# Optimization experiments

Hardware: AMD Instinct MI355X
Metric: run time of the kernel (lower is better)

## Reference

```python
import jax, jax.numpy as jnp
import numpy as np

B, T, C = 4, 2048, 1024  # n_embd == input_size == 1024
H, D = 16, 64            # num_heads, head_size


def setup_inputs() -> dict:
    key = jax.random.key(0)
    ks = jax.random.split(key, 5)
    s_in = (1.0 / C) ** 0.5   # ~Linear default init scale
    s_pr = (1.0 / (H * D)) ** 0.5
    return {
        "x": jax.random.normal(ks[0], (B, T, C), dtype=jnp.float32),
        "wq": jax.random.normal(ks[1], (H, C, D), dtype=jnp.float32) * s_in,
        "wk": jax.random.normal(ks[2], (H, C, D), dtype=jnp.float32) * s_in,
        "wv": jax.random.normal(ks[3], (H, C, D), dtype=jnp.float32) * s_in,
        "w_proj": jax.random.normal(ks[4], (H * D, C), dtype=jnp.float32) * s_pr,
        "b_proj": jnp.zeros((C,), dtype=jnp.float32),
    }


def reference(x, wq, wk, wv, w_proj, b_proj):
    Bb, Tt, Cc = x.shape
    # Batched per-head projections: [B,T,C] x [H,C,D] -> [B,H,T,D]
    q = jnp.einsum("btc,hcd->bhtd", x, wq)
    k = jnp.einsum("btc,hcd->bhtd", x, wk)
    v = jnp.einsum("btc,hcd->bhtd", x, wv)
    # NOTE: original scales by C**-0.5 with C = full embedding dim (quirk preserved)
    scale = Cc ** (-0.5)
    scores = jnp.einsum("bhtd,bhsd->bhts", q, k) * scale  # [B,H,T,T]
    causal = jnp.tril(jnp.ones((Tt, Tt), dtype=bool))
    scores = jnp.where(causal, scores, -jnp.inf)
    wei = jax.nn.softmax(scores, axis=-1)
    out = jnp.einsum("bhts,bhsd->bhtd", wei, v)           # [B,H,T,D]
    out = out.transpose(0, 2, 1, 3).reshape(Bb, Tt, -1)    # concat heads [B,T,H*D]
    return out @ w_proj + b_proj                           # [B,T,C]
```

## Files before the change

### kernel.cpp

```cpp
#include <hip/hip_runtime.h>
#include <stdint.h>


typedef uint32_t u32;
typedef __bf16 bf16x8 __attribute__((ext_vector_type(8)));
typedef __bf16 bf16x4 __attribute__((ext_vector_type(4)));
typedef unsigned short us8 __attribute__((ext_vector_type(8)));
typedef float f32x4 __attribute__((ext_vector_type(4)));

#define EXP2F(x) __builtin_amdgcn_exp2f(x)

static __device__ __forceinline__ unsigned short f2bf(float f) {
  union { float f; u32 i; } cv; cv.f = f;
  u32 x = cv.i;
  u32 r = (x + 0x7fffu + ((x >> 16) & 1u)) >> 16;
  return (unsigned short)r;
}

static __device__ __forceinline__ void gload_lds16(const unsigned short* g, unsigned short* l) {
  __builtin_amdgcn_global_load_lds(
      (__attribute__((address_space(1))) u32*)g,
      (__attribute__((address_space(3))) u32*)l, 16, 0, 0);
}

#define G8_LGKM do { asm volatile("s_waitcnt lgkmcnt(0)" ::: "memory"); \
                     __builtin_amdgcn_sched_barrier(0); } while (0)

__global__ __launch_bounds__(256) void cvt_f32_bf16(
    const float* __restrict__ src, unsigned short* __restrict__ dst) {
  size_t i = (size_t)(blockIdx.x * 256 + threadIdx.x) * 8u;
  float4 a = *(const float4*)(src + i);
  float4 b = *(const float4*)(src + i + 4);
  us8 v;
  v[0] = f2bf(a.x); v[1] = f2bf(a.y); v[2] = f2bf(a.z); v[3] = f2bf(a.w);
  v[4] = f2bf(b.x); v[5] = f2bf(b.y); v[6] = f2bf(b.z); v[7] = f2bf(b.w);
  *(us8*)(dst + i) = v;
}

__global__ __launch_bounds__(256) void transpose_qkv(
    const float* __restrict__ wq, const float* __restrict__ wk,
    const float* __restrict__ wv, unsigned short* __restrict__ dst) {
  __shared__ unsigned short lds[64][66];
  const float* src = (blockIdx.z == 0) ? wq : (blockIdx.z == 1) ? wk : wv;
  unsigned short* d = dst + ((size_t)blockIdx.z << 20);
  const int tid = threadIdx.x;
  const int h = blockIdx.y, c0 = blockIdx.x * 64;
  const float* s = src + (size_t)h * 65536u + (size_t)c0 * 64u;
#pragma unroll
  for (int it = 0; it < 16; ++it) {
    int idx = it * 256 + tid;
    int r = idx >> 6, dd = idx & 63;
    lds[dd][r] = f2bf(s[r * 64 + dd]);
  }
  __syncthreads();
#pragma unroll
  for (int it = 0; it < 16; ++it) {
    int idx = it * 256 + tid;
    int dd = idx >> 6, r = idx & 63;
    d[(size_t)(h * 64 + dd) * 1024u + c0 + r] = lds[dd][r];
  }
}

__global__ __launch_bounds__(256) void transpose_proj(
    const float* __restrict__ wp, unsigned short* __restrict__ dst) {
  __shared__ unsigned short lds[64][66];
  const int tid = threadIdx.x;
  const int c0 = blockIdx.x * 64, r0 = blockIdx.y * 64;
#pragma unroll
  for (int it = 0; it < 16; ++it) {
    int idx = it * 256 + tid;
    int r = idx >> 6, cc = idx & 63;
    lds[cc][r] = f2bf(wp[(size_t)(r0 + r) * 1024u + c0 + cc]);
  }
  __syncthreads();
#pragma unroll
  for (int it = 0; it < 16; ++it) {
    int idx = it * 256 + tid;
    int cc = idx >> 6, r = idx & 63;
    dst[(size_t)(c0 + cc) * 1024u + r0 + r] = lds[cc][r];
  }
}

__global__ __launch_bounds__(256) void transpose_v(
    const unsigned short* __restrict__ v, unsigned short* __restrict__ vt) {
  __shared__ unsigned short lds[64][66];
  const int tid = threadIdx.x;
  const int bh = blockIdx.y, t0 = blockIdx.x * 64;
  const unsigned short* src = v + ((size_t)(bh >> 4) * 2048 + t0) * 1024u + (bh & 15) * 64;
  unsigned short* dst = vt + (size_t)bh * 131072u + t0;
#pragma unroll
  for (int it = 0; it < 16; ++it) {
    int idx = it * 256 + tid;
    int r = idx >> 6, dd = idx & 63;
    lds[dd][r] = src[(size_t)r * 1024u + dd];
  }
  __syncthreads();
#pragma unroll
  for (int it = 0; it < 16; ++it) {
    int idx = it * 256 + tid;
    int dd = idx >> 6, r = idx & 63;
    dst[(size_t)dd * 2048u + r] = lds[dd][r];
  }
}

static __device__ __forceinline__ void gn_stage(const unsigned short* g,
                                                unsigned short* d, int tid) {
#pragma unroll
  for (int l = 0; l < 2; ++l) {
    int cid = l * 512 + tid;
    int r = cid >> 3, c = cid & 7;
    gload_lds16(g + (size_t)r * 1024 + ((c ^ (r & 7)) << 3), d + cid * 8);
  }
}
static __device__ __forceinline__ void gn_ldA(bf16x8 af[4][2], const unsigned short* As,
                                              int wr, int l15, int lhi) {
#pragma unroll
  for (int mi = 0; mi < 4; ++mi)
#pragma unroll
    for (int ks = 0; ks < 2; ++ks) {
      int row = wr * 64 + mi * 16 + l15;
      af[mi][ks] = *(const bf16x8*)(As + row * 64 + ((((ks << 2) | lhi) ^ (row & 7)) << 3));
    }
}
static __device__ __forceinline__ void gn_ldB(bf16x8 bf[2][2], const unsigned short* Bs,
                                              int wc, int np, int l15, int lhi) {
#pragma unroll
  for (int ni = 0; ni < 2; ++ni)
#pragma unroll
    for (int ks = 0; ks < 2; ++ks) {
      int row = wc * 64 + np * 32 + ni * 16 + l15;
      bf[ni][ks] = *(const bf16x8*)(Bs + row * 64 + ((((ks << 2) | lhi) ^ (row & 7)) << 3));
    }
}
static __device__ __forceinline__ void gn_quad(f32x4 acc[4][4], bf16x8 af[4][2],
                                               bf16x8 bf[2][2], int np) {
#pragma unroll
  for (int ks = 0; ks < 2; ++ks)
#pragma unroll
    for (int mi = 0; mi < 4; ++mi)
#pragma unroll
      for (int ni = 0; ni < 2; ++ni)
        acc[mi][np * 2 + ni] = __builtin_amdgcn_mfma_f32_16x16x32_bf16(
            af[mi][ks], bf[ni][ks], acc[mi][np * 2 + ni], 0, 0, 0);
}

template <int F32OUT>
__global__ __launch_bounds__(512, 2) void gemmN(
    const unsigned short* __restrict__ A, const unsigned short* __restrict__ Bt,
    const float* __restrict__ bias, void* __restrict__ Cv) {
  extern __shared__ __align__(16) unsigned short ldsm[];
  unsigned short* Ab = ldsm;
  unsigned short* Bb = ldsm + 16384;
  const int tid = threadIdx.x, wid = tid >> 6, lane = tid & 63;
  const int l15 = lane & 15, lhi = lane >> 4;
  const int wr = wid >> 2, wc = wid & 3;
  const int bid = blockIdx.x;
  const int mt = ((bid & 7) << 3) | ((bid >> 3) & 7);
  const int nt = bid >> 6;
  const int m0 = mt * 128, n0 = nt * 256;
  const unsigned short* Ag = A + (size_t)m0 * 1024;
  const unsigned short* Bg = Bt + (size_t)n0 * 1024;

  f32x4 acc[4][4] = {};
  bf16x8 af[4][2], b0[2][2], b1[2][2];

  gn_stage(Bg, Bb, tid);
  gn_stage(Bg + 128 * 1024, Bb + 8192, tid);
  gn_stage(Ag, Ab, tid);
  gn_stage(Ag + 64, Ab + 8192, tid);
  asm volatile("s_waitcnt vmcnt(2)" ::: "memory");
  __builtin_amdgcn_s_barrier();

  for (int j = 0; j < 8; ++j) {
    const bool last = (j == 7);
    const int kc = j * 128;
    gn_ldA(af, Ab, wr, l15, lhi);
    gn_ldB(b0, Bb, wc, 0, l15, lhi);
    gn_stage(Bg + (kc + 64), Bb + 16384, tid);
    gn_stage(Bg + 128 * 1024 + (kc + 64), Bb + 24576, tid);
    __builtin_amdgcn_s_barrier(); G8_LGKM;
    __builtin_amdgcn_s_setprio(1); gn_quad(acc, af, b0, 0); __builtin_amdgcn_s_setprio(0);
    __builtin_amdgcn_s_barrier();
    gn_ldB(b1, Bb, wc, 1, l15, lhi);
    if (!last) gn_stage(Ag + (kc + 128), Ab, tid);
    __builtin_amdgcn_s_barrier(); G8_LGKM;
    __builtin_amdgcn_s_setprio(1); gn_quad(acc, af, b1, 1); __builtin_amdgcn_s_setprio(0);
    if (last) { asm volatile("s_waitcnt vmcnt(0)" ::: "memory"); }
    else      { asm volatile("s_waitcnt vmcnt(2)" ::: "memory"); }
    __builtin_amdgcn_s_barrier();
    gn_ldA(af, Ab + 8192, wr, l15, lhi);
    gn_ldB(b0, Bb + 16384, wc, 0, l15, lhi);
    if (!last) {
      gn_stage(Bg + (kc + 128), Bb, tid);
      gn_stage(Bg + 128 * 1024 + (kc + 128), Bb + 8192, tid);
    }
    __builtin_amdgcn_s_barrier(); G8_LGKM;
    __builtin_amdgcn_s_setprio(1); gn_quad(acc, af, b0, 0); __builtin_amdgcn_s_setprio(0);
    __builtin_amdgcn_s_barrier();
    gn_ldB(b1, Bb + 16384, wc, 1, l15, lhi);
    if (!last) gn_stage(Ag + (kc + 192), Ab + 8192, tid);
    __builtin_amdgcn_s_barrier(); G8_LGKM;
    __builtin_amdgcn_s_setprio(1); gn_quad(acc, af, b1, 1); __builtin_amdgcn_s_setprio(0);
    if (!last) asm volatile("s_waitcnt vmcnt(2)" ::: "memory");
    __builtin_amdgcn_s_barrier();
  }

#pragma unroll
  for (int mi = 0; mi < 4; ++mi) {
#pragma unroll
    for (int ni = 0; ni < 4; ++ni) {
      const int n = n0 + wc * 64 + ni * 16 + l15;
      const int mr = m0 + wr * 64 + mi * 16 + lhi * 4;
      if constexpr (F32OUT) {
        float* O = (float*)Cv;
        const float b = bias[n];
#pragma unroll
        for (int r = 0; r < 4; ++r)
          O[(size_t)(mr + r) * 1024 + n] = acc[mi][ni][r] + b;
      } else {
        unsigned short* O = (unsigned short*)Cv + ((size_t)(n >> 10) << 23);
        const int nc = n & 1023;
#pragma unroll
        for (int r = 0; r < 4; ++r)
          O[(size_t)(mr + r) * 1024 + nc] = f2bf(acc[mi][ni][r]);
      }
    }
  }
}

#define QT 128
#define KVT 64
#define PSTR 72
#define SCLOG2E 0.04508422f
#define DTHR 128.0f

__global__ __launch_bounds__(512, 4) void attn_fwd(
    const unsigned short* __restrict__ Qg, const unsigned short* __restrict__ Kg,
    const unsigned short* __restrict__ Vtg, unsigned short* __restrict__ Og) {
  __shared__ __align__(16) unsigned short Kl[2][64 * 64];
  __shared__ __align__(16) unsigned short Vl[2][64 * 64];
  __shared__ __align__(16) unsigned short Pl[8][16 * PSTR];
  const int tid = threadIdx.x, wid = tid >> 6, lane = tid & 63;
  const int l15 = lane & 15, lhi = lane >> 4, x7 = lane & 7;
  const int bid = blockIdx.x;
  const int sub = bid & 63, pair = bid >> 6;
  const int bh = ((sub & 7) << 3) | (sub >> 3);
  const int qtA = pair, qtB = 15 - pair;
  const int n0 = 2 * (qtA + 1), n1 = 2 * (qtB + 1);
  const int ntot = n0 + n1;
  const size_t base = (size_t)(bh >> 4) * (2048u * 1024u) + (size_t)(bh & 15) * 64u;
  const size_t vtbase = (size_t)bh * 131072u;

  auto s0_of = [&](int g) { return ((g < n0) ? g : g - n0) * KVT; };

  auto stage = [&](int bufi, int s0) {
    int q = tid;
    int r = q >> 3;
    int c = (q & 7) ^ (r & 7);
    gload_lds16(Kg + base + (size_t)(s0 + r) * 1024u + c * 8, &Kl[bufi][q * 8]);
    gload_lds16(Vtg + vtbase + (size_t)r * 2048u + s0 + c * 8, &Vl[bufi][q * 8]);
  };

  stage(0, 0);
  __syncthreads();

  int g = 0;
  for (int pass = 0; pass < 2; ++pass) {
    const int qt = pass ? qtB : qtA;
    const int nt = pass ? n1 : n0;
    const int qrow0 = qt * QT + wid * 16;

    bf16x8 qf[2];
#pragma unroll
    for (int kj = 0; kj < 2; ++kj)
      qf[kj] = *(const bf16x8*)(Qg + base +
          (size_t)(qrow0 + l15) * 1024u + kj * 32 + lhi * 8);

    float mrun = -1e30f, lrun = 0.0f;
    f32x4 oacc[4] = {};

    for (int kt = 0; kt < nt; ++kt, ++g) {
      const int cur = g & 1;
      const int s0 = kt * KVT;
      if (g + 1 < ntot) stage(cur ^ 1, s0_of(g + 1));
      if (s0 <= qrow0 + 15) {
        const bool notfull = (s0 + KVT - 1 > qrow0);
        const unsigned short* Kb = Kl[cur];
        const unsigned short* Vb = Vl[cur];

        f32x4 sacc[4] = {};
#pragma unroll
        for (int kj = 0; kj < 2; ++kj) {
          bf16x8 kf[4];
#pragma unroll
          for (int sj = 0; sj < 4; ++sj) {
            int r = sj * 16 + l15;
            kf[sj] = *(const bf16x8*)(&Kb[r * 64 + (((kj * 4 + lhi) ^ x7) * 8)]);
          }
#pragma unroll
          for (int sj = 0; sj < 4; ++sj)
            sacc[sj] = __builtin_amdgcn_mfma_f32_16x16x32_bf16(
                kf[sj], qf[kj], sacc[sj], 0, 0, 0);
        }

        const int qa = qrow0 + l15;
        float mx = -3e38f;
        if (notfull) {
#pragma unroll
          for (int sj = 0; sj < 4; ++sj)
#pragma unroll
            for (int r = 0; r < 4; ++r) {
              int sa = s0 + sj * 16 + lhi * 4 + r;
              float v = (sa <= qa) ? sacc[sj][r] : -3e38f;
              sacc[sj][r] = v;
              mx = fmaxf(mx, v);
            }
        } else {
#pragma unroll
          for (int sj = 0; sj < 4; ++sj)
#pragma unroll
            for (int r = 0; r < 4; ++r)
              mx = fmaxf(mx, sacc[sj][r]);
        }
        mx = fmaxf(mx, __shfl_xor(mx, 16, 64));
        mx = fmaxf(mx, __shfl_xor(mx, 32, 64));

        if (__any(mx > mrun + DTHR)) {
          float mnew = fmaxf(mrun, mx);
          float sc = EXP2F((mrun - mnew) * SCLOG2E);
          mrun = mnew;
          lrun *= sc;
#pragma unroll
          for (int r = 0; r < 4; ++r) {
            float so = __shfl(sc, (lane & 48) + lhi * 4 + r, 64);
#pragma unroll
            for (int dj = 0; dj < 4; ++dj) oacc[dj][r] *= so;
          }
        }

        {
          const float m = mrun;
          float ps = 0.0f;
#pragma unroll
          for (int sj = 0; sj < 4; ++sj) {
            float p0 = EXP2F((sacc[sj][0] - m) * SCLOG2E);
            float p1 = EXP2F((sacc[sj][1] - m) * SCLOG2E);
            float p2 = EXP2F((sacc[sj][2] - m) * SCLOG2E);
            float p3 = EXP2F((sacc[sj][3] - m) * SCLOG2E);
            bf16x4 pk;
            pk[0] = (__bf16)p0; pk[1] = (__bf16)p1;
            pk[2] = (__bf16)p2; pk[3] = (__bf16)p3;
            *(bf16x4*)(&Pl[wid][l15 * PSTR + sj * 16 + lhi * 4]) = pk;
            ps += (p0 + p1) + (p2 + p3);
          }
          ps += __shfl_xor(ps, 16, 64);
          ps += __shfl_xor(ps, 32, 64);
          lrun += ps;
        }

#pragma unroll
        for (int kk = 0; kk < 2; ++kk) {
          bf16x8 pf, vf[4];
          pf = *(const bf16x8*)(&Pl[wid][l15 * PSTR + kk * 32 + lhi * 8]);
#pragma unroll
          for (int dj = 0; dj < 4; ++dj) {
            int r = dj * 16 + l15;
            vf[dj] = *(const bf16x8*)(&Vb[r * 64 + (((kk * 4 + lhi) ^ x7) * 8)]);
          }
#pragma unroll
          for (int dj = 0; dj < 4; ++dj)
            oacc[dj] = __builtin_amdgcn_mfma_f32_16x16x32_bf16(
                pf, vf[dj], oacc[dj], 0, 0, 0);
        }
      }

      __syncthreads();
    }

    float rn[4];
#pragma unroll
    for (int r = 0; r < 4; ++r)
      rn[r] = 1.0f / __shfl(lrun, (lane & 48) + lhi * 4 + r, 64);
#pragma unroll
    for (int dj = 0; dj < 4; ++dj)
#pragma unroll
      for (int r = 0; r < 4; ++r) {
        int t = qrow0 + lhi * 4 + r;
        Og[base + (size_t)t * 1024u + dj * 16 + l15] = f2bf(oacc[dj][r] * rn[r]);
      }
  }
}

extern "C" void kernel_launch(void* const* d_in, const int* in_sizes, int n_in,
                              void* d_out, int out_size, void* d_ws, size_t ws_size,
                              hipStream_t stream) {
  const float* x  = (const float*)d_in[0];
  const float* wq = (const float*)d_in[1];
  const float* wk = (const float*)d_in[2];
  const float* wv = (const float*)d_in[3];
  const float* wp = (const float*)d_in[4];
  const float* bp = (const float*)d_in[5];
  float* out = (float*)d_out;

  unsigned short* ws   = (unsigned short*)d_ws;
  unsigned short* x_bf = ws;
  unsigned short* wtq  = ws + ((size_t)8 << 20);
  unsigned short* wtp  = ws + ((size_t)11 << 20);
  unsigned short* qkv  = ws + ((size_t)12 << 20);
  unsigned short* q    = qkv;
  unsigned short* kk   = qkv + ((size_t)8 << 20);
  unsigned short* vv   = qkv + ((size_t)16 << 20);
  unsigned short* att  = vv;
  unsigned short* vt   = ws + ((size_t)36 << 20);

  (void)hipFuncSetAttribute(reinterpret_cast<const void*>(&gemmN<0>),
                            hipFuncAttributeMaxDynamicSharedMemorySize, 98304);
  (void)hipFuncSetAttribute(reinterpret_cast<const void*>(&gemmN<1>),
                            hipFuncAttributeMaxDynamicSharedMemorySize, 98304);

  cvt_f32_bf16<<<4096, 256, 0, stream>>>(x, x_bf);
  transpose_qkv<<<dim3(16, 16, 3), 256, 0, stream>>>(wq, wk, wv, wtq);
  transpose_proj<<<dim3(16, 16), 256, 0, stream>>>(wp, wtp);
  gemmN<0><<<768, 512, 98304, stream>>>(x_bf, wtq, nullptr, qkv);
  transpose_v<<<dim3(32, 64), 256, 0, stream>>>(vv, vt);
  attn_fwd<<<512, 512, 0, stream>>>(q, kk, vt, att);
  gemmN<1><<<256, 512, 98304, stream>>>(att, wtp, bp, out);
}
```

Measured before the change: 171.4 us.

## Merge prep kernels and compute softmax row sums via MFMA with ones

Folds the x conversion and the two weight-transpose kernels into one launch that dispatches on block index, removing two kernel launches. In attention, the softmax denominator is now accumulated by an extra MFMA of P against a ones vector, which replaces the per-tile shuffle reductions. The exponent argument is also folded into a single FMA, and the unmasked row max uses a tree reduction. This adds one MFMA per k-chunk and keeps four extra accumulator registers. The row sum is now taken over the bf16-rounded P rather than the fp32 values.

```diff
diff --git a/kernel.cpp b/kernel.cpp
--- a/kernel.cpp
+++ b/kernel.cpp
@@ -26,58 +26,61 @@
 #define G8_LGKM do { asm volatile("s_waitcnt lgkmcnt(0)" ::: "memory"); \
                      __builtin_amdgcn_sched_barrier(0); } while (0)
 
-__global__ __launch_bounds__(256) void cvt_f32_bf16(
-    const float* __restrict__ src, unsigned short* __restrict__ dst) {
-  size_t i = (size_t)(blockIdx.x * 256 + threadIdx.x) * 8u;
-  float4 a = *(const float4*)(src + i);
-  float4 b = *(const float4*)(src + i + 4);
-  us8 v;
-  v[0] = f2bf(a.x); v[1] = f2bf(a.y); v[2] = f2bf(a.z); v[3] = f2bf(a.w);
-  v[4] = f2bf(b.x); v[5] = f2bf(b.y); v[6] = f2bf(b.z); v[7] = f2bf(b.w);
-  *(us8*)(dst + i) = v;
-}
-
-__global__ __launch_bounds__(256) void transpose_qkv(
-    const float* __restrict__ wq, const float* __restrict__ wk,
-    const float* __restrict__ wv, unsigned short* __restrict__ dst) {
+__global__ __launch_bounds__(256) void prep(
+    const float* __restrict__ x, const float* __restrict__ wq,
+    const float* __restrict__ wk, const float* __restrict__ wv,
+    const float* __restrict__ wp, unsigned short* __restrict__ x_bf,
+    unsigned short* __restrict__ wtq, unsigned short* __restrict__ wtp) {
   __shared__ unsigned short lds[64][66];
-  const float* src = (blockIdx.z == 0) ? wq : (blockIdx.z == 1) ? wk : wv;
-  unsigned short* d = dst + ((size_t)blockIdx.z << 20);
-  const int tid = threadIdx.x;
-  const int h = blockIdx.y, c0 = blockIdx.x * 64;
-  const float* s = src + (size_t)h * 65536u + (size_t)c0 * 64u;
-#pragma unroll
-  for (int it = 0; it < 16; ++it) {
-    int idx = it * 256 + tid;
-    int r = idx >> 6, dd = idx & 63;
-    lds[dd][r] = f2bf(s[r * 64 + dd]);
-  }
-  __syncthreads();
-#pragma unroll
-  for (int it = 0; it < 16; ++it) {
-    int idx = it * 256 + tid;
-    int dd = idx >> 6, r = idx & 63;
-    d[(size_t)(h * 64 + dd) * 1024u + c0 + r] = lds[dd][r];
-  }
-}
-
-__global__ __launch_bounds__(256) void transpose_proj(
-    const float* __restrict__ wp, unsigned short* __restrict__ dst) {
-  __shared__ unsigned short lds[64][66];
-  const int tid = threadIdx.x;
-  const int c0 = blockIdx.x * 64, r0 = blockIdx.y * 64;
-#pragma unroll
-  for (int it = 0; it < 16; ++it) {
-    int idx = it * 256 + tid;
-    int r = idx >> 6, cc = idx & 63;
-    lds[cc][r] = f2bf(wp[(size_t)(r0 + r) * 1024u + c0 + cc]);
-  }
-  __syncthreads();
-#pragma unroll
-  for (int it = 0; it < 16; ++it) {
-    int idx = it * 256 + tid;
-    int cc = idx >> 6, r = idx & 63;
-    dst[(size_t)(c0 + cc) * 1024u + r0 + r] = lds[cc][r];
+  const int b = blockIdx.x, tid = threadIdx.x;
+  if (b < 4096) {
+    size_t i = (size_t)(b * 256 + tid) * 8u;
+    float4 a = *(const float4*)(x + i);
+    float4 c = *(const float4*)(x + i + 4);
+    us8 v;
+    v[0] = f2bf(a.x); v[1] = f2bf(a.y); v[2] = f2bf(a.z); v[3] = f2bf(a.w);
+    v[4] = f2bf(c.x); v[5] = f2bf(c.y); v[6] = f2bf(c.z); v[7] = f2bf(c.w);
+    *(us8*)(x_bf + i) = v;
+    return;
+  }
+  if (b < 4864) {
+    int idx = b - 4096;
+    int z = idx >> 8, rem = idx & 255;
+    int h = rem >> 4, c0 = (rem & 15) << 6;
+    const float* src = (z == 0) ? wq : (z == 1) ? wk : wv;
+    unsigned short* d = wtq + ((size_t)z << 20);
+    const float* s = src + (size_t)h * 65536u + (size_t)c0 * 64u;
+#pragma unroll
+    for (int it = 0; it < 16; ++it) {
+      int i2 = it * 256 + tid;
+      int r = i2 >> 6, dd = i2 & 63;
+      lds[dd][r] = f2bf(s[r * 64 + dd]);
+    }
+    __syncthreads();
+#pragma unroll
+    for (int it = 0; it < 16; ++it) {
+      int i2 = it * 256 + tid;
+      int dd = i2 >> 6, r = i2 & 63;
+      d[(size_t)(h * 64 + dd) * 1024u + c0 + r] = lds[dd][r];
+    }
+    return;
+  }
+  {
+    int idx = b - 4864;
+    int c0 = (idx >> 4) << 6, r0 = (idx & 15) << 6;
+#pragma unroll
+    for (int it = 0; it < 16; ++it) {
+      int i2 = it * 256 + tid;
+      int r = i2 >> 6, cc = i2 & 63;
+      lds[cc][r] = f2bf(wp[(size_t)(r0 + r) * 1024u + c0 + cc]);
+    }
+    __syncthreads();
+#pragma unroll
+    for (int it = 0; it < 16; ++it) {
+      int i2 = it * 256 + tid;
+      int cc = i2 >> 6, r = i2 & 63;
+      wtp[(size_t)(c0 + cc) * 1024u + r0 + r] = lds[cc][r];
+    }
   }
 }
 
@@ -251,6 +254,10 @@
   const size_t base = (size_t)(bh >> 4) * (2048u * 1024u) + (size_t)(bh & 15) * 64u;
   const size_t vtbase = (size_t)bh * 131072u;
 
+  bf16x8 vones;
+#pragma unroll
+  for (int j = 0; j < 8; ++j) vones[j] = (__bf16)1.0f;
+
   auto s0_of = [&](int g) { return ((g < n0) ? g : g - n0) * KVT; };
 
   auto stage = [&](int bufi, int s0) {
@@ -276,8 +283,9 @@
       qf[kj] = *(const bf16x8*)(Qg + base +
           (size_t)(qrow0 + l15) * 1024u + kj * 32 + lhi * 8);
 
-    float mrun = -1e30f, lrun = 0.0f;
+    float mrun = -1e30f;
     f32x4 oacc[4] = {};
+    f32x4 lacc = {};
 
     for (int kt = 0; kt < nt; ++kt, ++g) {
       const int cur = g & 1;
@@ -304,8 +312,9 @@
         }
 
         const int qa = qrow0 + l15;
-        float mx = -3e38f;
+        float mx;
         if (notfull) {
+          mx = -3e38f;
 #pragma unroll
           for (int sj = 0; sj < 4; ++sj)
 #pragma unroll
@@ -316,11 +325,11 @@
               mx = fmaxf(mx, v);
             }
         } else {
-#pragma unroll
-          for (int sj = 0; sj < 4; ++sj)
-#pragma unroll
-            for (int r = 0; r < 4; ++r)
-              mx = fmaxf(mx, sacc[sj][r]);
+          float m0a = fmaxf(fmaxf(sacc[0][0], sacc[0][1]), fmaxf(sacc[0][2], sacc[0][3]));
+          float m1a = fmaxf(fmaxf(sacc[1][0], sacc[1][1]), fmaxf(sacc[1][2], sacc[1][3]));
+          float m2a = fmaxf(fmaxf(sacc[2][0], sacc[2][1]), fmaxf(sacc[2][2], sacc[2][3]));
+          float m3a = fmaxf(fmaxf(sacc[3][0], sacc[3][1]), fmaxf(sacc[3][2], sacc[3][3]));
+          mx = fmaxf(fmaxf(m0a, m1a), fmaxf(m2a, m3a));
         }
         mx = fmaxf(mx, __shfl_xor(mx, 16, 64));
         mx = fmaxf(mx, __shfl_xor(mx, 32, 64));
@@ -329,33 +338,28 @@
           float mnew = fmaxf(mrun, mx);
           float sc = EXP2F((mrun - mnew) * SCLOG2E);
           mrun = mnew;
-          lrun *= sc;
 #pragma unroll
           for (int r = 0; r < 4; ++r) {
             float so = __shfl(sc, (lane & 48) + lhi * 4 + r, 64);
 #pragma unroll
             for (int dj = 0; dj < 4; ++dj) oacc[dj][r] *= so;
+            lacc[r] *= so;
           }
         }
 
         {
-          const float m = mrun;
-          float ps = 0.0f;
+          const float negmC = -mrun * SCLOG2E;
 #pragma unroll
           for (int sj = 0; sj < 4; ++sj) {
-            float p0 = EXP2F((sacc[sj][0] - m) * SCLOG2E);
-            float p1 = EXP2F((sacc[sj][1] - m) * SCLOG2E);
-            float p2 = EXP2F((sacc[sj][2] - m) * SCLOG2E);
-            float p3 = EXP2F((sacc[sj][3] - m) * SCLOG2E);
+            float p0 = EXP2F(__builtin_fmaf(sacc[sj][0], SCLOG2E, negmC));
+            float p1 = EXP2F(__builtin_fmaf(sacc[sj][1], SCLOG2E, negmC));
+            float p2 = EXP2F(__builtin_fmaf(sacc[sj][2], SCLOG2E, negmC));
+            float p3 = EXP2F(__builtin_fmaf(sacc[sj][3], SCLOG2E, negmC));
             bf16x4 pk;
             pk[0] = (__bf16)p0; pk[1] = (__bf16)p1;
             pk[2] = (__bf16)p2; pk[3] = (__bf16)p3;
             *(bf16x4*)(&Pl[wid][l15 * PSTR + sj * 16 + lhi * 4]) = pk;
-            ps += (p0 + p1) + (p2 + p3);
           }
-          ps += __shfl_xor(ps, 16, 64);
-          ps += __shfl_xor(ps, 32, 64);
-          lrun += ps;
         }
 
 #pragma unroll
@@ -371,6 +375,7 @@
           for (int dj = 0; dj < 4; ++dj)
             oacc[dj] = __builtin_amdgcn_mfma_f32_16x16x32_bf16(
                 pf, vf[dj], oacc[dj], 0, 0, 0);
+          lacc = __builtin_amdgcn_mfma_f32_16x16x32_bf16(pf, vones, lacc, 0, 0, 0);
         }
       }
 
@@ -379,8 +384,7 @@
 
     float rn[4];
 #pragma unroll
-    for (int r = 0; r < 4; ++r)
-      rn[r] = 1.0f / __shfl(lrun, (lane & 48) + lhi * 4 + r, 64);
+    for (int r = 0; r < 4; ++r) rn[r] = 1.0f / lacc[r];
 #pragma unroll
     for (int dj = 0; dj < 4; ++dj)
 #pragma unroll
@@ -418,9 +422,7 @@
   (void)hipFuncSetAttribute(reinterpret_cast<const void*>(&gemmN<1>),
                             hipFuncAttributeMaxDynamicSharedMemorySize, 98304);
 
-  cvt_f32_bf16<<<4096, 256, 0, stream>>>(x, x_bf);
-  transpose_qkv<<<dim3(16, 16, 3), 256, 0, stream>>>(wq, wk, wv, wtq);
-  transpose_proj<<<dim3(16, 16), 256, 0, stream>>>(wp, wtp);
+  prep<<<5120, 256, 0, stream>>>(x, wq, wk, wv, wp, x_bf, wtq, wtp);
   gemmN<0><<<768, 512, 98304, stream>>>(x_bf, wtq, nullptr, qkv);
   transpose_v<<<dim3(32, 64), 256, 0, stream>>>(vv, vt);
   attn_fwd<<<512, 512, 0, stream>>>(q, kk, vt, att);
```

Result: faster. 165.7 us (-3.3%).
